# Performance work log

Hardware: AMD Instinct MI355X
Metric: run time of the kernel (lower is better)

## Reference

```python
import jax, jax.numpy as jnp
import numpy as np

N_LEVELS = 16
F_PER_LEVEL = 2
TABLE_SIZE = 1 << 15          # 2**log2_hashmap_size
BASE_RES = 16
FINEST_RES = 512
PER_LEVEL_SCALE = (FINEST_RES / BASE_RES) ** (1.0 / (N_LEVELS - 1))
RANGE = np.pi                  # spherical coords live in [-pi, pi]
HASH_PRIME = np.uint32(2654435761)  # tcnn 2D hash prime (dim0 prime is 1)


def coord2sph(v):
    # unit vector -> (theta, phi): theta = acos(z) in [0, pi], phi = atan2(y, x) in [-pi, pi]
    theta = jnp.arccos(jnp.clip(v[..., 2], -1.0, 1.0))
    phi = jnp.arctan2(v[..., 1], v[..., 0])
    return jnp.stack([theta, phi], axis=-1)


def _normalize(v, eps=1e-12):
    # torch F.normalize: v / max(||v||, eps)
    n = jnp.linalg.norm(v, axis=-1, keepdims=True)
    return v / jnp.maximum(n, eps)


def hash_grid_encode(x01, table):
    """Instant-NGP style 2D multires hash encoding.
    x01: [N, 2] in [0, 1]; table: [L, T, F]. Returns [N, L*F]."""
    res = jnp.floor(BASE_RES * PER_LEVEL_SCALE ** jnp.arange(N_LEVELS)).astype(jnp.float32)  # [L]
    offs = jnp.array([[0, 0], [0, 1], [1, 0], [1, 1]], dtype=jnp.uint32)  # 4 corners
    offs_f = offs.astype(jnp.float32)

    def level(table_l, r):
        pos = x01 * r                      # [N,2]
        p0 = jnp.floor(pos)
        frac = pos - p0                    # [N,2]
        c = p0.astype(jnp.uint32)[:, None, :] + offs[None]          # [N,4,2]
        idx = (c[..., 0] ^ (c[..., 1] * HASH_PRIME)) % jnp.uint32(TABLE_SIZE)  # [N,4]
        feats = table_l[idx]               # [N,4,F] irregular gather
        w = jnp.prod(jnp.where(offs_f[None] > 0, frac[:, None, :], 1.0 - frac[:, None, :]), axis=-1)  # [N,4]
        return jnp.einsum('nc,ncf->nf', w, feats)  # [N,F]

    out = jax.vmap(level, in_axes=(0, 0), out_axes=1)(table, res)  # [N,L,F]
    return out.reshape(x01.shape[0], N_LEVELS * F_PER_LEVEL)


def setup_inputs() -> dict:
    key = jax.random.key(0)
    k1, k2, k3 = jax.random.split(key, 3)
    x = jax.random.normal(k1, (1048576, 6), dtype=jnp.float32)
    table1 = jax.random.uniform(k2, (N_LEVELS, TABLE_SIZE, F_PER_LEVEL), jnp.float32, -1e-4, 1e-4)
    table2 = jax.random.uniform(k3, (N_LEVELS, TABLE_SIZE, F_PER_LEVEL), jnp.float32, -1e-4, 1e-4)
    return {"x": x, "table1": table1, "table2": table2}


def reference(x, table1, table2):
    origin = x[:, :3]
    d = _normalize(x[:, 3:] - origin)                    # ray direction
    sph_d = (coord2sph(d) + RANGE) / (2.0 * RANGE)       # -> [0,1]^2
    hash_dir = hash_grid_encode(sph_d, table1)           # [N, 32]
    vect = jnp.cross(d, jnp.cross(origin, d))            # perpendicular foot vector
    sph_v = (coord2sph(_normalize(vect)) + RANGE) / (2.0 * RANGE)
    hash_vect = hash_grid_encode(sph_v, table2)          # [N, 32]
    return jnp.concatenate([vect, hash_dir, hash_vect], axis=-1)  # [N, 67]
```

## Files before the change

kernel.cpp:

```cpp
#include <hip/hip_runtime.h>
#include <math.h>

#define HASH_PRIME 2654435761u
#define TMASK 32767u
#define NPB 128
#define HSTRIDE 68
#define CHUNK 65536

typedef float vf2 __attribute__((ext_vector_type(2)));
typedef float vf4 __attribute__((ext_vector_type(4)));
typedef unsigned vu2 __attribute__((ext_vector_type(2)));

__device__ __forceinline__ unsigned pack_bf16(float a, float b) {
    return (__float_as_uint(a) >> 16) | (__float_as_uint(b) & 0xffff0000u);
}
__device__ __forceinline__ float bf_lo(unsigned w) { return __uint_as_float(w << 16); }
__device__ __forceinline__ float bf_hi(unsigned w) { return __uint_as_float(w & 0xffff0000u); }

__global__ __launch_bounds__(256)
void prepass(const float* __restrict__ x,
             unsigned* __restrict__ cD, unsigned* __restrict__ cV,
             vf4* __restrict__ vect, int n)
{
    const int i = blockIdx.x * 256 + threadIdx.x;
    if (i >= n) return;
    const float* xi = x + (long long)i * 6;
    vf2 p0 = __builtin_nontemporal_load((const vf2*)(xi + 0));
    vf2 p1 = __builtin_nontemporal_load((const vf2*)(xi + 2));
    vf2 p2 = __builtin_nontemporal_load((const vf2*)(xi + 4));
    float ox = p0.x, oy = p0.y, oz = p1.x;
    float dx = p1.y - ox, dy = p2.x - oy, dz = p2.y - oz;

    float nd = sqrtf(dx * dx + dy * dy + dz * dz);
    float invd = 1.0f / fmaxf(nd, 1e-12f);
    dx *= invd; dy *= invd; dz *= invd;

    float th_d = acosf(fminf(fmaxf(dz, -1.f), 1.f));
    float ph_d = atan2f(dy, dx);
    float u_d = (th_d + 3.14159265358979323846f) / 6.28318530717958647692f;
    float v_d = (ph_d + 3.14159265358979323846f) / 6.28318530717958647692f;

    float cx = oy * dz - oz * dy;
    float cy = oz * dx - ox * dz;
    float cz = ox * dy - oy * dx;
    float vx = dy * cz - dz * cy;
    float vy = dz * cx - dx * cz;
    float vz = dx * cy - dy * cx;

    float nv = sqrtf(vx * vx + vy * vy + vz * vz);
    float invv = 1.0f / fmaxf(nv, 1e-12f);
    float wx = vx * invv, wy = vy * invv, wz = vz * invv;
    float th_v = acosf(fminf(fmaxf(wz, -1.f), 1.f));
    float ph_v = atan2f(wy, wx);
    float u_v = (th_v + 3.14159265358979323846f) / 6.28318530717958647692f;
    float v_v = (ph_v + 3.14159265358979323846f) / 6.28318530717958647692f;

    unsigned ud = (unsigned)fminf(fmaxf(u_d, 0.f) * 65536.f, 65535.f);
    unsigned vd = (unsigned)fminf(fmaxf(v_d, 0.f) * 65536.f, 65535.f);
    unsigned uv = (unsigned)fminf(fmaxf(u_v, 0.f) * 65536.f, 65535.f);
    unsigned vv_ = (unsigned)fminf(fmaxf(v_v, 0.f) * 65536.f, 65535.f);
    __builtin_nontemporal_store(ud | (vd << 16), &cD[i]);
    __builtin_nontemporal_store(uv | (vv_ << 16), &cV[i]);
    vf4 vo; vo.x = vx; vo.y = vy; vo.z = vz; vo.w = 0.f;
    __builtin_nontemporal_store(vo, &vect[i]);
}

__device__ __forceinline__ unsigned enc_point(const unsigned* __restrict__ tl,
                                              float rs, unsigned cw)
{
    float pu = (float)(cw & 0xffffu) * rs;
    float pv = (float)(cw >> 16) * rs;
    float fu = floorf(pu), fv = floorf(pv);
    float au = pu - fu, av = pv - fv;
    unsigned cu = (unsigned)fu, cv = (unsigned)fv;
    unsigned h0 = cv * HASH_PRIME;
    unsigned h1 = (cv + 1u) * HASH_PRIME;
    unsigned w00 = tl[(cu ^ h0) & TMASK];
    unsigned w01 = tl[(cu ^ h1) & TMASK];
    unsigned w10 = tl[((cu + 1u) ^ h0) & TMASK];
    unsigned w11 = tl[((cu + 1u) ^ h1) & TMASK];
    float a00 = (1.f - au) * (1.f - av);
    float a01 = (1.f - au) * av;
    float a10 = au * (1.f - av);
    float a11 = au * av;
    float o0 = a00 * bf_lo(w00) + a01 * bf_lo(w01) + a10 * bf_lo(w10) + a11 * bf_lo(w11);
    float o1 = a00 * bf_hi(w00) + a01 * bf_hi(w01) + a10 * bf_hi(w10) + a11 * bf_hi(w11);
    return pack_bf16(o0, o1);
}

template<bool FULL>
__global__ __launch_bounds__(1024)
void stageA(const float* __restrict__ t1, const float* __restrict__ t2,
            const unsigned* __restrict__ cD, const unsigned* __restrict__ cV,
            unsigned* __restrict__ F, int n)
{
    __shared__ unsigned tl[32768];
    const int tb = blockIdx.y;
    const float resv[16] = {16.f, 20.f, 25.f, 32.f, 40.f, 50.f, 64.f, 80.f,
                            101.f, 128.f, 161.f, 203.f, 256.f, 322.f, 406.f, 512.f};
    const float rs = resv[tb & 15] * (1.f / 65536.f);
    const float* src = (tb < 16) ? (t1 + (size_t)tb * 65536)
                                 : (t2 + (size_t)(tb - 16) * 65536);
    const vf4* src4 = (const vf4*)src;
    vu2* tl2 = (vu2*)tl;
    #pragma unroll
    for (int j = 0; j < 16; ++j) {
        const int k = j * 1024 + threadIdx.x;
        vf4 e = src4[k];
        vu2 w; w.x = pack_bf16(e.x, e.y); w.y = pack_bf16(e.z, e.w);
        tl2[k] = w;
    }
    __syncthreads();

    const unsigned* cc = (tb < 16) ? cD : cV;
    unsigned* Fo = F + (size_t)tb * (size_t)n;
    const int ibase = blockIdx.x * CHUNK + threadIdx.x;

    if (FULL) {
        #pragma unroll 2
        for (int k = 0; k < CHUNK / 1024; k += 4) {
            const int i0 = ibase + (k + 0) * 1024;
            const int i1 = ibase + (k + 1) * 1024;
            const int i2 = ibase + (k + 2) * 1024;
            const int i3 = ibase + (k + 3) * 1024;
            unsigned c0 = cc[i0];
            unsigned c1 = cc[i1];
            unsigned c2 = cc[i2];
            unsigned c3 = cc[i3];
            unsigned r0 = enc_point(tl, rs, c0);
            unsigned r1 = enc_point(tl, rs, c1);
            unsigned r2 = enc_point(tl, rs, c2);
            unsigned r3 = enc_point(tl, rs, c3);
            Fo[i0] = r0;
            Fo[i1] = r1;
            Fo[i2] = r2;
            Fo[i3] = r3;
        }
    } else {
        #pragma unroll 4
        for (int k = 0; k < CHUNK / 1024; ++k) {
            const int i = ibase + k * 1024;
            if (i < n) {
                unsigned c = cc[i];
                Fo[i] = enc_point(tl, rs, c);
            }
        }
    }
}

__global__ __launch_bounds__(NPB)
void stageB(const unsigned* __restrict__ F, const vf4* __restrict__ vect,
            float* __restrict__ out, int n)
{
    __shared__ unsigned hlds[NPB * (HSTRIDE / 2)];
    __shared__ float vlds[NPB * 4];
    const int tid = threadIdx.x;
    const long long i = (long long)blockIdx.x * NPB + tid;
    if (i < (long long)n) {
        vf4 vv = vect[i];
        vlds[tid * 4 + 0] = vv.x;
        vlds[tid * 4 + 1] = vv.y;
        vlds[tid * 4 + 2] = vv.z;
        unsigned* hrow = &hlds[tid * (HSTRIDE / 2)];
        #pragma unroll
        for (int c = 0; c < 32; ++c)
            hrow[c] = F[(size_t)c * (size_t)n + i];
    }
    __syncthreads();

    const long long blk_start = (long long)blockIdx.x * NPB;
    const int rows = (int)(((blk_start + NPB) <= (long long)n) ? NPB : (n - blk_start));
    if (rows <= 0) return;
    const long long base = blk_start * 67ll;
    const int total = rows * 67;
    const unsigned short* hs = (const unsigned short*)hlds;
    for (int k = tid; k < total; k += NPB) {
        const int r = k / 67;
        const int c = k - r * 67;
        float val;
        if (c < 3) {
            val = vlds[r * 4 + c];
        } else {
            unsigned hv = (unsigned)hs[r * HSTRIDE + (c - 3)];
            val = __uint_as_float(hv << 16);
        }
        __builtin_nontemporal_store(val, &out[base + k]);
    }
}

__device__ __forceinline__ void enc_level_f32(const float* __restrict__ tbl,
                                              float u, float v, float r,
                                              float& o0, float& o1)
{
    float pu = u * r, pv = v * r;
    float fu = floorf(pu), fv = floorf(pv);
    float au = pu - fu, av = pv - fv;
    unsigned cu = (unsigned)fu, cv = (unsigned)fv;
    unsigned h0 = cv * HASH_PRIME;
    unsigned h1 = (cv + 1u) * HASH_PRIME;
    unsigned i00 = (cu ^ h0) & TMASK;
    unsigned i01 = (cu ^ h1) & TMASK;
    unsigned i10 = ((cu + 1u) ^ h0) & TMASK;
    unsigned i11 = ((cu + 1u) ^ h1) & TMASK;
    vf2 g00 = *(const vf2*)(tbl + 2u * i00);
    vf2 g01 = *(const vf2*)(tbl + 2u * i01);
    vf2 g10 = *(const vf2*)(tbl + 2u * i10);
    vf2 g11 = *(const vf2*)(tbl + 2u * i11);
    float w00 = (1.f - au) * (1.f - av);
    float w01 = (1.f - au) * av;
    float w10 = au * (1.f - av);
    float w11 = au * av;
    o0 = w00 * g00.x + w01 * g01.x + w10 * g10.x + w11 * g11.x;
    o1 = w00 * g00.y + w01 * g01.y + w10 * g10.y + w11 * g11.y;
}

__global__ __launch_bounds__(NPB)
void hashprif_fallback(const float* __restrict__ x,
                       const float* __restrict__ t1,
                       const float* __restrict__ t2,
                       float* __restrict__ out,
                       int n)
{
    __shared__ unsigned hlds[NPB * (HSTRIDE / 2)];
    __shared__ float vlds[NPB * 4];
    const float res[16] = {16.f, 20.f, 25.f, 32.f, 40.f, 50.f, 64.f, 80.f,
                           101.f, 128.f, 161.f, 203.f, 256.f, 322.f, 406.f, 512.f};
    const int tid = threadIdx.x;
    const long long i = (long long)blockIdx.x * NPB + tid;
    const bool valid = i < (long long)n;

    if (valid) {
        const float* xi = x + i * 6ll;
        vf2 p0 = __builtin_nontemporal_load((const vf2*)(xi + 0));
        vf2 p1 = __builtin_nontemporal_load((const vf2*)(xi + 2));
        vf2 p2 = __builtin_nontemporal_load((const vf2*)(xi + 4));
        float ox = p0.x, oy = p0.y, oz = p1.x;
        float dx = p1.y - ox, dy = p2.x - oy, dz = p2.y - oz;
        float nd = sqrtf(dx * dx + dy * dy + dz * dz);
        float invd = 1.0f / fmaxf(nd, 1e-12f);
        dx *= invd; dy *= invd; dz *= invd;
        float th_d = acosf(fminf(fmaxf(dz, -1.f), 1.f));
        float ph_d = atan2f(dy, dx);
        float u_d = (th_d + 3.14159265358979323846f) / 6.28318530717958647692f;
        float v_d = (ph_d + 3.14159265358979323846f) / 6.28318530717958647692f;
        float cx = oy * dz - oz * dy;
        float cy = oz * dx - ox * dz;
        float cz = ox * dy - oy * dx;
        float vx = dy * cz - dz * cy;
        float vy = dz * cx - dx * cz;
        float vz = dx * cy - dy * cx;
        float nv = sqrtf(vx * vx + vy * vy + vz * vz);
        float invv = 1.0f / fmaxf(nv, 1e-12f);
        float wx = vx * invv, wy = vy * invv, wz = vz * invv;
        float th_v = acosf(fminf(fmaxf(wz, -1.f), 1.f));
        float ph_v = atan2f(wy, wx);
        float u_v = (th_v + 3.14159265358979323846f) / 6.28318530717958647692f;
        float v_v = (ph_v + 3.14159265358979323846f) / 6.28318530717958647692f;
        vlds[tid * 4 + 0] = vx;
        vlds[tid * 4 + 1] = vy;
        vlds[tid * 4 + 2] = vz;
        unsigned* hrow = &hlds[tid * (HSTRIDE / 2)];
        #pragma unroll
        for (int l = 0; l < 16; ++l) {
            float f0, f1;
            enc_level_f32(t1 + (size_t)l * 65536, u_d, v_d, res[l], f0, f1);
            hrow[l] = pack_bf16(f0, f1);
        }
        #pragma unroll
        for (int l = 0; l < 16; ++l) {
            float g0, g1;
            enc_level_f32(t2 + (size_t)l * 65536, u_v, v_v, res[l], g0, g1);
            hrow[16 + l] = pack_bf16(g0, g1);
        }
    }
    __syncthreads();
    const long long blk_start = (long long)blockIdx.x * NPB;
    const int rows = (int)(((blk_start + NPB) <= (long long)n) ? NPB : (n - blk_start));
    if (rows <= 0) return;
    const long long base = blk_start * 67ll;
    const int total = rows * 67;
    const unsigned short* hs = (const unsigned short*)hlds;
    for (int k = tid; k < total; k += NPB) {
        const int r = k / 67;
        const int c = k - r * 67;
        float val;
        if (c < 3) val = vlds[r * 4 + c];
        else {
            unsigned hv = (unsigned)hs[r * HSTRIDE + (c - 3)];
            val = __uint_as_float(hv << 16);
        }
        __builtin_nontemporal_store(val, &out[base + k]);
    }
}

extern "C" void kernel_launch(void* const* d_in, const int* in_sizes, int n_in,
                              void* d_out, int out_size, void* d_ws, size_t ws_size,
                              hipStream_t stream) {
    const float* x  = (const float*)d_in[0];
    const float* t1 = (const float*)d_in[1];
    const float* t2 = (const float*)d_in[2];
    float* out = (float*)d_out;
    const int n = in_sizes[0] / 6;
    const size_t nn = (size_t)n;
    const size_t need = 152ull * nn;

    if (ws_size >= need) {
        unsigned* cD = (unsigned*)d_ws;
        unsigned* cV = cD + nn;
        vf4* vect = (vf4*)((char*)d_ws + 8ull * nn);
        unsigned* F = (unsigned*)((char*)d_ws + 24ull * nn);
        hipLaunchKernelGGL(prepass, dim3((n + 255) / 256), dim3(256), 0, stream,
                           x, cD, cV, vect, n);
        dim3 ga((n + CHUNK - 1) / CHUNK, 32);
        if (n % CHUNK == 0) {
            hipLaunchKernelGGL(HIP_KERNEL_NAME(stageA<true>), ga, dim3(1024), 0, stream,
                               t1, t2, cD, cV, F, n);
        } else {
            hipLaunchKernelGGL(HIP_KERNEL_NAME(stageA<false>), ga, dim3(1024), 0, stream,
                               t1, t2, cD, cV, F, n);
        }
        hipLaunchKernelGGL(stageB, dim3((n + NPB - 1) / NPB), dim3(NPB), 0, stream,
                           F, vect, out, n);
    } else {
        hipLaunchKernelGGL(hashprif_fallback, dim3((n + NPB - 1) / NPB), dim3(NPB), 0, stream,
                           x, t1, t2, out, n);
    }
}
```

Measured before the change: 156.9 us.

## Pre-pack bf16 tables once, double stageA chunk, vectorize stageB output stores

The prepass kernel gets 32 extra blocks that convert each level's fp32 table into packed bf16 words in workspace. StageA blocks can then copy the packed table straight into LDS instead of each block re-reading fp32 and converting. CHUNK is doubled so fewer blocks each pay the table-load cost, which also reduces parallelism to 8x32 blocks. StageB changes the LDS row stride and writes output as 16-byte vector nontemporal stores, with a scalar tail loop, in place of scalar stores.

```diff
diff --git a/kernel.cpp b/kernel.cpp
--- a/kernel.cpp
+++ b/kernel.cpp
@@ -4,8 +4,9 @@
 #define HASH_PRIME 2654435761u
 #define TMASK 32767u
 #define NPB 128
+#define HWORDS 35
 #define HSTRIDE 68
-#define CHUNK 65536
+#define CHUNK 131072
 
 typedef float vf2 __attribute__((ext_vector_type(2)));
 typedef float vf4 __attribute__((ext_vector_type(4)));
@@ -19,9 +20,27 @@
 
 __global__ __launch_bounds__(256)
 void prepass(const float* __restrict__ x,
+             const float* __restrict__ t1, const float* __restrict__ t2,
              unsigned* __restrict__ cD, unsigned* __restrict__ cV,
-             vf4* __restrict__ vect, int n)
-{
+             vf4* __restrict__ vect, unsigned* __restrict__ Tp,
+             int n, int nbp)
+{
+    if ((int)blockIdx.x >= nbp) {
+        const int tb = (int)blockIdx.x - nbp;
+        const float* src = (tb < 16) ? (t1 + (size_t)tb * 65536)
+                                     : (t2 + (size_t)(tb - 16) * 65536);
+        const vf4* s4 = (const vf4*)src;
+        vu2* dst = (vu2*)(Tp + (size_t)tb * 32768);
+        #pragma unroll 8
+        for (int j = 0; j < 64; ++j) {
+            const int k = j * 256 + (int)threadIdx.x;
+            vf4 e = s4[k];
+            vu2 w; w.x = pack_bf16(e.x, e.y); w.y = pack_bf16(e.z, e.w);
+            dst[k] = w;
+        }
+        return;
+    }
+
     const int i = blockIdx.x * 256 + threadIdx.x;
     if (i >= n) return;
     const float* xi = x + (long long)i * 6;
@@ -88,9 +107,10 @@
     return pack_bf16(o0, o1);
 }
 
-template<bool FULL>
+template<bool FULL, bool PACKED>
 __global__ __launch_bounds__(1024)
 void stageA(const float* __restrict__ t1, const float* __restrict__ t2,
+            const unsigned* __restrict__ Tp,
             const unsigned* __restrict__ cD, const unsigned* __restrict__ cV,
             unsigned* __restrict__ F, int n)
 {
@@ -99,16 +119,27 @@
     const float resv[16] = {16.f, 20.f, 25.f, 32.f, 40.f, 50.f, 64.f, 80.f,
                             101.f, 128.f, 161.f, 203.f, 256.f, 322.f, 406.f, 512.f};
     const float rs = resv[tb & 15] * (1.f / 65536.f);
-    const float* src = (tb < 16) ? (t1 + (size_t)tb * 65536)
-                                 : (t2 + (size_t)(tb - 16) * 65536);
-    const vf4* src4 = (const vf4*)src;
-    vu2* tl2 = (vu2*)tl;
-    #pragma unroll
-    for (int j = 0; j < 16; ++j) {
-        const int k = j * 1024 + threadIdx.x;
-        vf4 e = src4[k];
-        vu2 w; w.x = pack_bf16(e.x, e.y); w.y = pack_bf16(e.z, e.w);
-        tl2[k] = w;
+
+    if constexpr (PACKED) {
+        const vf4* s4 = (const vf4*)(Tp + (size_t)tb * 32768);
+        vf4* tl4 = (vf4*)tl;
+        #pragma unroll
+        for (int j = 0; j < 8; ++j) {
+            const int k = j * 1024 + threadIdx.x;
+            tl4[k] = s4[k];
+        }
+    } else {
+        const float* src = (tb < 16) ? (t1 + (size_t)tb * 65536)
+                                     : (t2 + (size_t)(tb - 16) * 65536);
+        const vf4* src4 = (const vf4*)src;
+        vu2* tl2 = (vu2*)tl;
+        #pragma unroll
+        for (int j = 0; j < 16; ++j) {
+            const int k = j * 1024 + threadIdx.x;
+            vf4 e = src4[k];
+            vu2 w; w.x = pack_bf16(e.x, e.y); w.y = pack_bf16(e.z, e.w);
+            tl2[k] = w;
+        }
     }
     __syncthreads();
 
@@ -152,39 +183,51 @@
 void stageB(const unsigned* __restrict__ F, const vf4* __restrict__ vect,
             float* __restrict__ out, int n)
 {
-    __shared__ unsigned hlds[NPB * (HSTRIDE / 2)];
+    __shared__ unsigned hlds[NPB * HWORDS];
     __shared__ float vlds[NPB * 4];
     const int tid = threadIdx.x;
-    const long long i = (long long)blockIdx.x * NPB + tid;
+    const long long blk_start = (long long)blockIdx.x * NPB;
+    const long long i = blk_start + tid;
     if (i < (long long)n) {
         vf4 vv = vect[i];
         vlds[tid * 4 + 0] = vv.x;
         vlds[tid * 4 + 1] = vv.y;
         vlds[tid * 4 + 2] = vv.z;
-        unsigned* hrow = &hlds[tid * (HSTRIDE / 2)];
+        unsigned* hrow = &hlds[tid * HWORDS];
         #pragma unroll
         for (int c = 0; c < 32; ++c)
             hrow[c] = F[(size_t)c * (size_t)n + i];
     }
     __syncthreads();
 
-    const long long blk_start = (long long)blockIdx.x * NPB;
     const int rows = (int)(((blk_start + NPB) <= (long long)n) ? NPB : (n - blk_start));
     if (rows <= 0) return;
     const long long base = blk_start * 67ll;
     const int total = rows * 67;
     const unsigned short* hs = (const unsigned short*)hlds;
-    for (int k = tid; k < total; k += NPB) {
-        const int r = k / 67;
-        const int c = k - r * 67;
-        float val;
-        if (c < 3) {
-            val = vlds[r * 4 + c];
-        } else {
-            unsigned hv = (unsigned)hs[r * HSTRIDE + (c - 3)];
-            val = __uint_as_float(hv << 16);
-        }
-        __builtin_nontemporal_store(val, &out[base + k]);
+
+    const int nq = total >> 2;
+    vf4* out4 = (vf4*)(out + base);
+    for (int k = tid; k < nq; k += NPB) {
+        vf4 o;
+        #pragma unroll
+        for (int j = 0; j < 4; ++j) {
+            const int e = 4 * k + j;
+            const int r = e / 67;
+            const int c = e - r * 67;
+            float val;
+            if (c < 3) val = vlds[r * 4 + c];
+            else       val = __uint_as_float((unsigned)hs[r * (2 * HWORDS) + (c - 3)] << 16);
+            o[j] = val;
+        }
+        __builtin_nontemporal_store(o, &out4[k]);
+    }
+    for (int e = (nq << 2) + tid; e < total; e += NPB) {
+        const int r = e / 67;
+        const int c = e - r * 67;
+        float val = (c < 3) ? vlds[r * 4 + c]
+                            : __uint_as_float((unsigned)hs[r * (2 * HWORDS) + (c - 3)] << 16);
+        __builtin_nontemporal_store(val, &out[base + e]);
     }
 }
 
@@ -302,22 +345,38 @@
     float* out = (float*)d_out;
     const int n = in_sizes[0] / 6;
     const size_t nn = (size_t)n;
-    const size_t need = 152ull * nn;
-
-    if (ws_size >= need) {
+    const size_t base_need = 152ull * nn;
+    const size_t tp_bytes  = 32ull * 32768ull * 4ull;
+    const size_t need_packed = base_need + tp_bytes;
+
+    if (ws_size >= base_need) {
         unsigned* cD = (unsigned*)d_ws;
         unsigned* cV = cD + nn;
         vf4* vect = (vf4*)((char*)d_ws + 8ull * nn);
         unsigned* F = (unsigned*)((char*)d_ws + 24ull * nn);
-        hipLaunchKernelGGL(prepass, dim3((n + 255) / 256), dim3(256), 0, stream,
-                           x, cD, cV, vect, n);
+        const bool packed = (ws_size >= need_packed);
+        unsigned* Tp = packed ? (unsigned*)((char*)d_ws + base_need) : (unsigned*)nullptr;
+
+        const int nbp = (n + 255) / 256;
+        const int gpre = packed ? (nbp + 32) : nbp;
+        hipLaunchKernelGGL(prepass, dim3(gpre), dim3(256), 0, stream,
+                           x, t1, t2, cD, cV, vect, Tp, n, nbp);
+
         dim3 ga((n + CHUNK - 1) / CHUNK, 32);
         if (n % CHUNK == 0) {
-            hipLaunchKernelGGL(HIP_KERNEL_NAME(stageA<true>), ga, dim3(1024), 0, stream,
-                               t1, t2, cD, cV, F, n);
+            if (packed)
+                hipLaunchKernelGGL(HIP_KERNEL_NAME(stageA<true, true>), ga, dim3(1024), 0, stream,
+                                   t1, t2, Tp, cD, cV, F, n);
+            else
+                hipLaunchKernelGGL(HIP_KERNEL_NAME(stageA<true, false>), ga, dim3(1024), 0, stream,
+                                   t1, t2, Tp, cD, cV, F, n);
         } else {
-            hipLaunchKernelGGL(HIP_KERNEL_NAME(stageA<false>), ga, dim3(1024), 0, stream,
-                               t1, t2, cD, cV, F, n);
+            if (packed)
+                hipLaunchKernelGGL(HIP_KERNEL_NAME(stageA<false, true>), ga, dim3(1024), 0, stream,
+                                   t1, t2, Tp, cD, cV, F, n);
+            else
+                hipLaunchKernelGGL(HIP_KERNEL_NAME(stageA<false, false>), ga, dim3(1024), 0, stream,
+                                   t1, t2, Tp, cD, cV, F, n);
         }
         hipLaunchKernelGGL(stageB, dim3((n + NPB - 1) / NPB), dim3(NPB), 0, stream,
                            F, vect, out, n);
```

Result: no change. 159.4 us (+1.6%).
